# Performance work log

Measured on AMD Instinct MI355X. Metric: run time of the kernel, lower is better.

## Reference

```python
import jax, jax.numpy as jnp
import numpy as np
from jax import lax

RES = 14
DIM = 384
KEY_DIM = 32
NUM_HEADS = 12
ATTN_RATIO = 4
NH_KD = KEY_DIM * NUM_HEADS            # 384
DH = ATTN_RATIO * KEY_DIM * NUM_HEADS  # 1536
HQKV = DH + 2 * NH_KD                  # 2304
BN_EPS = 1e-5


def _bias_idxs():
    ys, xs = np.meshgrid(np.arange(RES), np.arange(RES), indexing='ij')
    ys = ys.reshape(-1); xs = xs.reshape(-1)
    dy = np.abs(ys[:, None] - ys[None, :])
    dx = np.abs(xs[:, None] - xs[None, :])
    return jnp.asarray(dy * RES + dx, dtype=jnp.int32)  # [196,196], 196 unique offsets


def setup_inputs() -> dict:
    key = jax.random.key(0)
    ks = jax.random.split(key, 16)
    B = 128
    x = jax.random.normal(ks[0], (B, DIM, RES, RES), dtype=jnp.float32)
    # qkv: 1x1 conv DIM->HQKV + BN
    qkv_w = jax.random.normal(ks[1], (HQKV, DIM, 1, 1), dtype=jnp.float32) * 0.05
    qkv_g = jax.random.normal(ks[2], (HQKV,), dtype=jnp.float32) * 0.1 + 1.0
    qkv_b = jax.random.normal(ks[3], (HQKV,), dtype=jnp.float32) * 0.1
    qkv_m = jax.random.normal(ks[4], (HQKV,), dtype=jnp.float32) * 0.1
    qkv_v = jax.random.uniform(ks[5], (HQKV,), dtype=jnp.float32) + 0.5
    # dw: depthwise 3x3 conv on q channels + BN
    dw_w = jax.random.normal(ks[6], (NH_KD, 1, 3, 3), dtype=jnp.float32) * 0.2
    dw_g = jax.random.normal(ks[7], (NH_KD,), dtype=jnp.float32) * 0.1 + 1.0
    dw_b = jax.random.normal(ks[8], (NH_KD,), dtype=jnp.float32) * 0.1
    dw_m = jax.random.normal(ks[9], (NH_KD,), dtype=jnp.float32) * 0.1
    dw_v = jax.random.uniform(ks[10], (NH_KD,), dtype=jnp.float32) + 0.5
    # proj: ReLU -> 1x1 conv DH->DIM + BN
    proj_w = jax.random.normal(ks[11], (DIM, DH, 1, 1), dtype=jnp.float32) * 0.05
    proj_g = jax.random.normal(ks[12], (DIM,), dtype=jnp.float32) * 0.1 + 1.0
    proj_b = jax.random.normal(ks[13], (DIM,), dtype=jnp.float32) * 0.1
    proj_m = jax.random.normal(ks[14], (DIM,), dtype=jnp.float32) * 0.1
    proj_v = jax.random.uniform(ks[15], (DIM,), dtype=jnp.float32) + 0.5
    ab = jax.random.normal(jax.random.fold_in(key, 99), (NUM_HEADS, RES * RES), dtype=jnp.float32) * 0.1
    return {
        'x': x,
        'qkv_w': qkv_w, 'qkv_g': qkv_g, 'qkv_b': qkv_b, 'qkv_m': qkv_m, 'qkv_v': qkv_v,
        'dw_w': dw_w, 'dw_g': dw_g, 'dw_b': dw_b, 'dw_m': dw_m, 'dw_v': dw_v,
        'proj_w': proj_w, 'proj_g': proj_g, 'proj_b': proj_b, 'proj_m': proj_m, 'proj_v': proj_v,
        'attn_biases': ab,
        'bias_idxs': _bias_idxs(),
    }


def _bn(x, g, b, m, v):
    scale = g / jnp.sqrt(v + BN_EPS)
    return x * scale[None, :, None, None] + (b - m * scale)[None, :, None, None]


def reference(x, qkv_w, qkv_g, qkv_b, qkv_m, qkv_v,
              dw_w, dw_g, dw_b, dw_m, dw_v,
              proj_w, proj_g, proj_b, proj_m, proj_v,
              attn_biases, bias_idxs):
    B, _, H, W = x.shape
    n = H * W
    scale = KEY_DIM ** -0.5
    # 1x1 conv + BN
    qkv = jnp.einsum('bchw,oc->bohw', x, qkv_w[:, :, 0, 0])
    qkv = _bn(qkv, qkv_g, qkv_b, qkv_m, qkv_v)
    q = qkv[:, :NH_KD]
    k = qkv[:, NH_KD:2 * NH_KD]
    v = qkv[:, 2 * NH_KD:]
    # depthwise 3x3 conv + BN on q
    q = lax.conv_general_dilated(q, dw_w, (1, 1), ((1, 1), (1, 1)),
                                 dimension_numbers=('NCHW', 'OIHW', 'NCHW'),
                                 feature_group_count=NH_KD)
    q = _bn(q, dw_g, dw_b, dw_m, dw_v)
    # heads: [b, h, d, n]
    q = q.reshape(B, NUM_HEADS, KEY_DIM, n)
    k = k.reshape(B, NUM_HEADS, KEY_DIM, n)
    v = v.reshape(B, NUM_HEADS, ATTN_RATIO * KEY_DIM, n)
    bias = attn_biases[:, bias_idxs]  # [h, n, n]
    attn = jnp.einsum('bhdn,bhdm->bhnm', q, k) * scale + bias[None]
    attn = jax.nn.softmax(attn, axis=-1)
    out = jnp.einsum('bhdm,bhnm->bhdn', v, attn).reshape(B, DH, H, W)
    out = jax.nn.relu(out)
    out = jnp.einsum('bchw,oc->bohw', out, proj_w[:, :, 0, 0])
    return _bn(out, proj_g, proj_b, proj_m, proj_v)
```

## Files before the change

kernel.cpp:

```cpp
#include <hip/hip_runtime.h>

typedef __bf16 bf16;
typedef bf16 bf16x8 __attribute__((ext_vector_type(8)));
typedef bf16 bf16x4 __attribute__((ext_vector_type(4)));
typedef short short4v __attribute__((ext_vector_type(4)));
typedef float f32x4 __attribute__((ext_vector_type(4)));

#define NPIX 196
#define CIN 384
#define NHEADS 12
#define MPAD 224
#define VSTRIDE 232
#define OSTRIDE 40
#define TSTRIDE 136

__device__ __forceinline__ float ldf(const void* p, size_t i, int f) {
    return f ? ((const float*)p)[i] : (float)((const bf16*)p)[i];
}

__device__ __forceinline__ void gld16(const void* g, void* lds_wave_base) {
    __builtin_amdgcn_global_load_lds(
        (const __attribute__((address_space(1))) void*)(unsigned long long)g,
        (__attribute__((address_space(3))) void*)(unsigned long long)lds_wave_base,
        16, 0, 0);
}

__device__ __forceinline__ int xcd_swizzle(int orig, int nwg) {
    int q = nwg >> 3, r = nwg & 7;
    int xcd = orig & 7, idx = orig >> 3;
    return (xcd < r ? xcd * (q + 1) : r * (q + 1) + (xcd - r) * q) + idx;
}

__device__ __forceinline__ f32x4 mfma16(bf16x4 a, bf16x4 b, f32x4 c) {
#if __has_builtin(__builtin_amdgcn_mfma_f32_16x16x16bf16_1k)
    return __builtin_amdgcn_mfma_f32_16x16x16bf16_1k(
        __builtin_bit_cast(short4v, a), __builtin_bit_cast(short4v, b), c, 0, 0, 0);
#else
    asm volatile("v_mfma_f32_16x16x16_bf16 %0, %1, %2, %0" : "+v"(c) : "v"(a), "v"(b));
    return c;
#endif
}

__device__ __forceinline__ f32x4 vmax4(f32x4 a, f32x4 b) {
    f32x4 r;
    r[0] = fmaxf(a[0], b[0]);
    r[1] = fmaxf(a[1], b[1]);
    r[2] = fmaxf(a[2], b[2]);
    r[3] = fmaxf(a[3], b[3]);
    return r;
}

__global__ void detect_kernel(const unsigned int* __restrict__ x, int* __restrict__ flag) {
    __shared__ int cnt;
    if (threadIdx.x == 0) cnt = 0;
    __syncthreads();
    int c = 0;
#pragma unroll
    for (int k = 0; k < 8; k++) {
        unsigned int w = x[threadIdx.x * 8 + k];
        unsigned int e = (w >> 7) & 0xFFu;
        if (e > 200u) c++;
    }
    atomicAdd(&cnt, c);
    __syncthreads();
    if (threadIdx.x == 0) *flag = (cnt >= 16) ? 1 : 0;
}

__global__ void convert_kernel(const void* __restrict__ src, bf16* __restrict__ dst, int n,
                               const int* __restrict__ flag) {
    int f = *flag;
    for (int i = blockIdx.x * 256 + threadIdx.x; i < n; i += gridDim.x * 256)
        dst[i] = (bf16)ldf(src, i, f);
}

__global__ void transpose_x_kernel(const void* __restrict__ x, const int* __restrict__ flag,
                                   bf16* __restrict__ xt, int b0) {
    __shared__ bf16 tile[32][33];
    int f = *flag;
    int b = blockIdx.z, gb = b0 + b;
    int c0 = blockIdx.y * 32;
    int hw0 = blockIdx.x * 32;
    int tx = threadIdx.x, ty = threadIdx.y;
    int hw = hw0 + tx, c = c0 + ty;
    if (hw < NPIX) tile[ty][tx] = (bf16)ldf(x, ((size_t)gb * CIN + c) * NPIX + hw, f);
    __syncthreads();
    int hw2 = hw0 + ty, c2 = c0 + tx;
    if (hw2 < NPIX) xt[((size_t)b * NPIX + hw2) * CIN + c2] = tile[tx][ty];
}

__device__ __forceinline__ void gemm_tile(const bf16* __restrict__ A, const bf16* __restrict__ B,
                                          int K, bf16* smem, f32x4 acc[4][4]) {
    int tid = threadIdx.x;
    int wave = tid >> 6, lane = tid & 63;
    int wm = wave >> 1, wn = wave & 1;
    int row = lane & 15, grp = lane >> 4;
    int sr = lane >> 3;
    int scg = (lane & 7) ^ sr;
    const int BUF = 128 * 64;
    bf16* As = smem;
    bf16* Bs = smem + 2 * BUF;
    const bf16* Ag = A + (size_t)(wave * 8 + sr) * K + scg * 8;
    const bf16* Bg = B + (size_t)(wave * 8 + sr) * K + scg * 8;
#pragma unroll
    for (int p = 0; p < 4; p++) {
        gld16(Ag + (size_t)(p * 32) * K, As + (p * 256 + wave * 64) * 8);
        gld16(Bg + (size_t)(p * 32) * K, Bs + (p * 256 + wave * 64) * 8);
    }
    int cur = 0;
#pragma unroll 1
    for (int kb = 0; kb < K; kb += 64) {
        if (kb + 64 < K) {
            bf16* Asn = As + (cur ^ 1) * BUF;
            bf16* Bsn = Bs + (cur ^ 1) * BUF;
#pragma unroll
            for (int p = 0; p < 4; p++) {
                gld16(Ag + (size_t)(p * 32) * K + kb + 64, Asn + (p * 256 + wave * 64) * 8);
                gld16(Bg + (size_t)(p * 32) * K + kb + 64, Bsn + (p * 256 + wave * 64) * 8);
            }
            __builtin_amdgcn_sched_barrier(0);
            asm volatile("s_waitcnt vmcnt(8)" ::: "memory");
        } else {
            __builtin_amdgcn_sched_barrier(0);
            asm volatile("s_waitcnt vmcnt(0)" ::: "memory");
        }
        __builtin_amdgcn_s_barrier();
        __builtin_amdgcn_sched_barrier(0);
        const bf16* Asc = As + cur * BUF;
        const bf16* Bsc = Bs + cur * BUF;
#pragma unroll
        for (int ki = 0; ki < 2; ki++) {
            bf16x8 af[4], bfr[4];
#pragma unroll
            for (int t = 0; t < 4; t++) {
                int ra = wm * 64 + t * 16 + row;
                af[t] = *(const bf16x8*)(Asc + ra * 64 + (((ki * 4 + grp) ^ (ra & 7)) * 8));
                int rb = wn * 64 + t * 16 + row;
                bfr[t] = *(const bf16x8*)(Bsc + rb * 64 + (((ki * 4 + grp) ^ (rb & 7)) * 8));
            }
#pragma unroll
            for (int mt = 0; mt < 4; mt++)
#pragma unroll
                for (int nt = 0; nt < 4; nt++)
                    acc[mt][nt] =
                        __builtin_amdgcn_mfma_f32_16x16x32_bf16(af[mt], bfr[nt], acc[mt][nt], 0, 0, 0);
        }
        __builtin_amdgcn_sched_barrier(0);
        __builtin_amdgcn_s_barrier();
        cur ^= 1;
    }
    __builtin_amdgcn_sched_barrier(0);
}

__global__ __launch_bounds__(256) void gemm_qkv_kernel(
    const bf16* __restrict__ xt, const bf16* __restrict__ w,
    const void* __restrict__ g, const void* __restrict__ bb,
    const void* __restrict__ mm, const void* __restrict__ vv, const int* __restrict__ flag,
    bf16* __restrict__ qb, bf16* __restrict__ kt, bf16* __restrict__ vb) {
    __shared__ bf16 smem[4 * 128 * 64];
    f32x4 acc[4][4];
#pragma unroll
    for (int i = 0; i < 4; i++)
#pragma unroll
        for (int j = 0; j < 4; j++) acc[i][j] = (f32x4){0.f, 0.f, 0.f, 0.f};
    int nwg = gridDim.x * gridDim.y;
    int l = xcd_swizzle(blockIdx.y * gridDim.x + blockIdx.x, nwg);
    int m0 = (l % gridDim.x) * 128, n0 = (l / gridDim.x) * 128;
    gemm_tile(w + (size_t)m0 * CIN, xt + (size_t)n0 * CIN, CIN, smem, acc);
    int f = *flag;
    int tid = threadIdx.x;
    int wave = tid >> 6, lane = tid & 63;
    int wm = wave >> 1, wn = wave & 1, row = lane & 15, grp = lane >> 4;
    if (m0 >= 384 && m0 < 768) {
        bf16* tbuf = smem;
#pragma unroll
        for (int mt = 0; mt < 4; mt++) {
#pragma unroll
            for (int r = 0; r < 4; r++) {
                int ol = wm * 64 + mt * 16 + grp * 4 + r;
                int o = m0 + ol;
                float scv = ldf(g, o, f) * rsqrtf(ldf(vv, o, f) + 1e-5f);
                float sh = ldf(bb, o, f) - ldf(mm, o, f) * scv;
#pragma unroll
                for (int nt = 0; nt < 4; nt++) {
                    int nl = wn * 64 + nt * 16 + row;
                    tbuf[nl * TSTRIDE + ol] = (bf16)(acc[mt][nt][r] * scv + sh);
                }
            }
        }
        __syncthreads();
#pragma unroll
        for (int it = 0; it < 8; it++) {
            int g2 = it * 256 + tid;
            int nl = g2 >> 4, ch = g2 & 15;
            *(bf16x8*)(kt + (size_t)(n0 + nl) * CIN + (m0 - 384) + ch * 8) =
                *(const bf16x8*)(tbuf + nl * TSTRIDE + ch * 8);
        }
    } else {
#pragma unroll
        for (int mt = 0; mt < 4; mt++) {
#pragma unroll
            for (int r = 0; r < 4; r++) {
                int o = m0 + wm * 64 + mt * 16 + grp * 4 + r;
                float scv = ldf(g, o, f) * rsqrtf(ldf(vv, o, f) + 1e-5f);
                float sh = ldf(bb, o, f) - ldf(mm, o, f) * scv;
#pragma unroll
                for (int nt = 0; nt < 4; nt++) {
                    int n = n0 + wn * 64 + nt * 16 + row;
                    int b = n / NPIX, hw = n - b * NPIX;
                    float val = acc[mt][nt][r] * scv + sh;
                    bf16 bv = (bf16)val;
                    if (o < 384) {
                        qb[((size_t)b * 384 + o) * NPIX + hw] = bv;
                    } else {
                        vb[((size_t)b * 1536 + (o - 768)) * MPAD + hw] = bv;
                    }
                }
            }
        }
    }
}

__global__ __launch_bounds__(256) void gemm_proj_kernel(
    const bf16* __restrict__ ot, const bf16* __restrict__ w,
    const void* __restrict__ g, const void* __restrict__ bb,
    const void* __restrict__ mm, const void* __restrict__ vv, const int* __restrict__ flag,
    void* __restrict__ out, int b0) {
    __shared__ bf16 smem[4 * 128 * 64];
    f32x4 acc[4][4];
#pragma unroll
    for (int i = 0; i < 4; i++)
#pragma unroll
        for (int j = 0; j < 4; j++) acc[i][j] = (f32x4){0.f, 0.f, 0.f, 0.f};
    int nwg = gridDim.x * gridDim.y;
    int l = xcd_swizzle(blockIdx.y * gridDim.x + blockIdx.x, nwg);
    int m0 = (l % gridDim.x) * 128, n0 = (l / gridDim.x) * 128;
    gemm_tile(w + (size_t)m0 * 1536, ot + (size_t)n0 * 1536, 1536, smem, acc);
    int f = *flag;
    int wave = threadIdx.x >> 6, lane = threadIdx.x & 63;
    int wm = wave >> 1, wn = wave & 1, row = lane & 15, grp = lane >> 4;
#pragma unroll
    for (int mt = 0; mt < 4; mt++) {
#pragma unroll
        for (int r = 0; r < 4; r++) {
            int o = m0 + wm * 64 + mt * 16 + grp * 4 + r;
            float scv = ldf(g, o, f) * rsqrtf(ldf(vv, o, f) + 1e-5f);
            float sh = ldf(bb, o, f) - ldf(mm, o, f) * scv;
#pragma unroll
            for (int nt = 0; nt < 4; nt++) {
                int n = n0 + wn * 64 + nt * 16 + row;
                int b = n / NPIX, hw = n - b * NPIX;
                float val = acc[mt][nt][r] * scv + sh;
                size_t oidx = ((size_t)(b0 + b) * 384 + o) * NPIX + hw;
                if (f) ((float*)out)[oidx] = val;
                else ((bf16*)out)[oidx] = (bf16)val;
            }
        }
    }
}

__global__ void dwconv_kernel(const bf16* __restrict__ qb, const bf16* __restrict__ w,
                              const void* __restrict__ g, const void* __restrict__ bb,
                              const void* __restrict__ mm, const void* __restrict__ vv,
                              const int* __restrict__ flag, bf16* __restrict__ qt) {
    __shared__ bf16 tile[32][33];
    int f = *flag;
    int b = blockIdx.z;
    int c0 = blockIdx.y * 32, hw0 = blockIdx.x * 32;
    int tx = threadIdx.x, ty = threadIdx.y;
    int c = c0 + ty, hw = hw0 + tx;
    if (hw < NPIX) {
        int y = hw / 14, x = hw % 14;
        float acc = 0.f;
        const bf16* wp = w + c * 9;
        const bf16* qp = qb + ((size_t)b * 384 + c) * NPIX;
#pragma unroll
        for (int ky = 0; ky < 3; ky++) {
            int yy = y + ky - 1;
            if (yy < 0 || yy >= 14) continue;
#pragma unroll
            for (int kx = 0; kx < 3; kx++) {
                int xx = x + kx - 1;
                if (xx < 0 || xx >= 14) continue;
                acc += (float)qp[yy * 14 + xx] * (float)wp[ky * 3 + kx];
            }
        }
        float sc = ldf(g, c, f) * rsqrtf(ldf(vv, c, f) + 1e-5f);
        float sh = ldf(bb, c, f) - ldf(mm, c, f) * sc;
        tile[ty][tx] = (bf16)(acc * sc + sh);
    }
    __syncthreads();
    int hw2 = hw0 + ty, c2 = c0 + tx;
    if (hw2 < NPIX) qt[((size_t)b * NPIX + hw2) * CIN + c2] = tile[tx][ty];
}

__global__ void bias_gather_kernel(const void* __restrict__ ab, const int* __restrict__ idx,
                                   const int* __restrict__ flag, float* __restrict__ biasf) {
    int f = *flag;
    int t = blockIdx.x * 256 + threadIdx.x;
    if (t >= NHEADS * NPIX * MPAD) return;
    int h = t / (NPIX * MPAD);
    int rem = t - h * (NPIX * MPAD);
    int n = rem / MPAD, m = rem - n * MPAD;
    biasf[t] = (m < NPIX) ? ldf(ab, h * NPIX + idx[n * NPIX + m], f) : -1e30f;
}

__global__ void zero_vpad_kernel(bf16* __restrict__ vb, int rows) {
    int t = blockIdx.x * 256 + threadIdx.x;
    if (t >= rows * 7) return;
    int r = t / 7, c = t - r * 7;
    *(unsigned long long*)(vb + (size_t)r * MPAD + NPIX + c * 4) = 0ull;
}

__global__ __launch_bounds__(256, 2) void attn_kernel(
    const bf16* __restrict__ qt, const bf16* __restrict__ ktp, const bf16* __restrict__ vb,
    const float* __restrict__ biasf, bf16* __restrict__ ot) {
    __shared__ bf16 Vs[128 * VSTRIDE];
    __shared__ bf16 Osh[4][16 * OSTRIDE];
    int nwg = gridDim.x * gridDim.y;
    int l = xcd_swizzle(blockIdx.y * gridDim.x + blockIdx.x, nwg);
    int h = l % NHEADS, b = l / NHEADS;
    int tid = threadIdx.x;
    int wave = tid >> 6, lane = tid & 63;
    int row = lane & 15, grp = lane >> 4;
    const float scale = 0.17677669529663687f;
    const f32x4 zf = {0.f, 0.f, 0.f, 0.f};

    {
        const bf16* vsrc = vb + ((size_t)b * 1536 + h * 128) * MPAD;
#pragma unroll
        for (int it = 0; it < 14; it++) {
            int i = it * 256 + tid;
            int r = i / 28, gch = i - r * 28;
            *(bf16x8*)(Vs + r * VSTRIDE + gch * 8) = *(const bf16x8*)(vsrc + (size_t)i * 8);
        }
    }
    __syncthreads();

    const bf16* vls = Vs + row * VSTRIDE + grp * 4;

    for (int nb = wave; nb < 13; nb += 4) {
        int n0 = nb * 16;
        int n = n0 + row;
        int nc = n > 195 ? 195 : n;

        bf16x8 aq = *(const bf16x8*)(qt + ((size_t)b * NPIX + nc) * CIN + h * 32 + grp * 8);

        f32x4 sacc[14];
#pragma unroll
        for (int mt = 0; mt < 14; mt++) {
            int krow = mt * 16 + row;
            if (krow > 195) krow = 195;
            bf16x8 ak = *(const bf16x8*)(ktp + ((size_t)b * NPIX + krow) * CIN + h * 32 + grp * 8);
            sacc[mt] = __builtin_amdgcn_mfma_f32_16x16x32_bf16(ak, aq, zf, 0, 0, 0);
        }

        const float* bp = biasf + ((size_t)h * NPIX + nc) * MPAD + grp * 4;
        f32x4 mxv = {-3.4e38f, -3.4e38f, -3.4e38f, -3.4e38f};
#pragma unroll
        for (int mt = 0; mt < 14; mt++) {
            f32x4 bv = *(const f32x4*)(bp + mt * 16);
            f32x4 s = sacc[mt] * scale + bv;
            sacc[mt] = s;
            mxv = vmax4(mxv, s);
        }
        float mx = fmaxf(fmaxf(mxv[0], mxv[1]), fmaxf(mxv[2], mxv[3]));
        mx = fmaxf(mx, __shfl_xor(mx, 16));
        mx = fmaxf(mx, __shfl_xor(mx, 32));

        f32x4 sumv = zf;
        bf16x4 pf[14];
#pragma unroll
        for (int mt = 0; mt < 14; mt++) {
            f32x4 e;
#pragma unroll
            for (int r = 0; r < 4; r++) e[r] = __expf(sacc[mt][r] - mx);
            sumv += e;
            bf16x4 pb;
#pragma unroll
            for (int r = 0; r < 4; r++) pb[r] = (bf16)e[r];
            pf[mt] = pb;
        }
        float sum = (sumv[0] + sumv[1]) + (sumv[2] + sumv[3]);
        sum += __shfl_xor(sum, 16);
        sum += __shfl_xor(sum, 32);
        float inv = 1.f / sum;

        f32x4 oacc[8];
#pragma unroll
        for (int dt = 0; dt < 8; dt++) oacc[dt] = zf;
#pragma unroll
        for (int mt = 0; mt < 14; mt++) {
            bf16x4 p = pf[mt];
#pragma unroll
            for (int dt = 0; dt < 8; dt++) {
                bf16x4 v4 = *(const bf16x4*)(vls + dt * 16 * VSTRIDE + mt * 16);
                oacc[dt] = mfma16(v4, p, oacc[dt]);
            }
        }

        bf16* osw = Osh[wave];
        int r2 = lane >> 2, c2 = lane & 3;
        int n2 = n0 + r2;
        bf16* op = ot + ((size_t)b * NPIX + n2) * 1536 + h * 128;
#pragma unroll
        for (int dp = 0; dp < 4; dp++) {
#pragma unroll
            for (int u = 0; u < 2; u++) {
                int dt = dp * 2 + u;
                bf16x4 o4;
#pragma unroll
                for (int r = 0; r < 4; r++) {
                    float v = oacc[dt][r] * inv;
                    o4[r] = (bf16)(v > 0.f ? v : 0.f);
                }
                *(bf16x4*)(osw + row * OSTRIDE + u * 16 + grp * 4) = o4;
            }
            asm volatile("s_waitcnt lgkmcnt(0)" ::: "memory");
            if (n2 < NPIX) {
                bf16x8 ov = *(const bf16x8*)(osw + r2 * OSTRIDE + c2 * 8);
                *(bf16x8*)(op + dp * 32 + c2 * 8) = ov;
            }
            asm volatile("s_waitcnt lgkmcnt(0)" ::: "memory");
        }
    }
}

extern "C" void kernel_launch(void* const* d_in, const int* in_sizes, int n_in,
                              void* d_out, int out_size, void* d_ws, size_t ws_size,
                              hipStream_t stream) {
    const void* x      = d_in[0];
    const void* qkv_w  = d_in[1];
    const void* qkv_g  = d_in[2];
    const void* qkv_b  = d_in[3];
    const void* qkv_m  = d_in[4];
    const void* qkv_v  = d_in[5];
    const void* dw_w   = d_in[6];
    const void* dw_g   = d_in[7];
    const void* dw_b   = d_in[8];
    const void* dw_m   = d_in[9];
    const void* dw_v   = d_in[10];
    const void* proj_w = d_in[11];
    const void* proj_g = d_in[12];
    const void* proj_b = d_in[13];
    const void* proj_m = d_in[14];
    const void* proj_v = d_in[15];
    const void* ab     = d_in[16];
    const int*  idx    = (const int*)d_in[17];

    char* ws = (char*)d_ws;
    size_t off = 0;
    auto alloc = [&](size_t bytes) { void* p = ws + off; off += (bytes + 255) & ~(size_t)255; return p; };

    int*   flag = (int*)alloc(4);
    bf16*  wq   = (bf16*)alloc((size_t)2304 * 384 * 2);
    bf16*  wp   = (bf16*)alloc((size_t)384 * 1536 * 2);
    bf16*  wd   = (bf16*)alloc((size_t)384 * 9 * 2);
    float* biasf= (float*)alloc((size_t)NHEADS * NPIX * MPAD * 4);
    size_t fixed = off;

    const size_t s_xt = (size_t)NPIX * CIN;
    const size_t s_qb = (size_t)384 * NPIX;
    const size_t s_kt = (size_t)NPIX * 384;
    const size_t s_vb = (size_t)1536 * MPAD;
    const size_t s_ot = (size_t)NPIX * 1536;
    const size_t per_image = (s_xt + s_qb + s_kt + s_vb + s_ot) * 2;

    int CB = 128;
    while (CB > 32 && fixed + (size_t)CB * per_image > ws_size) CB >>= 1;

    bf16* xt  = (bf16*)alloc((size_t)CB * s_xt * 2);
    bf16* qb  = (bf16*)alloc((size_t)CB * s_qb * 2);
    bf16* ktp = (bf16*)alloc((size_t)CB * s_kt * 2);
    bf16* vb  = (bf16*)alloc((size_t)CB * s_vb * 2);
    bf16* ot  = (bf16*)alloc((size_t)CB * s_ot * 2);
    bf16* qt  = xt;

    detect_kernel<<<dim3(1), dim3(256), 0, stream>>>((const unsigned int*)x, flag);
    convert_kernel<<<dim3(256), dim3(256), 0, stream>>>(qkv_w, wq, 2304 * 384, flag);
    convert_kernel<<<dim3(256), dim3(256), 0, stream>>>(proj_w, wp, 384 * 1536, flag);
    convert_kernel<<<dim3(4), dim3(256), 0, stream>>>(dw_w, wd, 384 * 9, flag);
    int bg = (NHEADS * NPIX * MPAD + 255) / 256;
    bias_gather_kernel<<<dim3(bg), dim3(256), 0, stream>>>(ab, idx, flag, biasf);
    int vrows = CB * 1536;
    zero_vpad_kernel<<<dim3((vrows * 7 + 255) / 256), dim3(256), 0, stream>>>(vb, vrows);

    dim3 tb(32, 32);
    for (int b0 = 0; b0 < 128; b0 += CB) {
        int cb = (128 - b0 < CB) ? (128 - b0) : CB;
        int ntiles = (cb * NPIX) / 128;
        transpose_x_kernel<<<dim3(7, 12, cb), tb, 0, stream>>>(x, flag, xt, b0);
        gemm_qkv_kernel<<<dim3(18, ntiles), dim3(256), 0, stream>>>(xt, wq, qkv_g, qkv_b, qkv_m,
                                                                    qkv_v, flag, qb, ktp, vb);
        dwconv_kernel<<<dim3(7, 12, cb), tb, 0, stream>>>(qb, wd, dw_g, dw_b, dw_m, dw_v, flag, qt);
        attn_kernel<<<dim3(NHEADS, cb), dim3(256), 0, stream>>>(qt, ktp, vb, biasf, ot);
        gemm_proj_kernel<<<dim3(3, ntiles), dim3(256), 0, stream>>>(ot, wp, proj_g, proj_b, proj_m,
                                                                    proj_v, flag, d_out, b0);
    }
}
```

Baseline: 446.9 us.

## Merge prep kernels, stage GEMM epilogues through LDS, add MFMA priority hints

```diff
diff --git a/kernel.cpp b/kernel.cpp
--- a/kernel.cpp
+++ b/kernel.cpp
@@ -13,6 +13,12 @@
 #define VSTRIDE 232
 #define OSTRIDE 40
 #define TSTRIDE 136
+#define TSF 136
+
+#define N_WQ (2304 * 384)
+#define N_WP (384 * 1536)
+#define N_WD (384 * 9)
+#define N_BI (NHEADS * NPIX * MPAD)
 
 __device__ __forceinline__ float ldf(const void* p, size_t i, int f) {
     return f ? ((const float*)p)[i] : (float)((const bf16*)p)[i];
@@ -66,11 +72,31 @@
     if (threadIdx.x == 0) *flag = (cnt >= 16) ? 1 : 0;
 }
 
-__global__ void convert_kernel(const void* __restrict__ src, bf16* __restrict__ dst, int n,
-                               const int* __restrict__ flag) {
+__global__ void prep_kernel(const void* __restrict__ qkv_w, const void* __restrict__ proj_w,
+                            const void* __restrict__ dw_w, const void* __restrict__ ab,
+                            const int* __restrict__ idx, const int* __restrict__ flag,
+                            bf16* __restrict__ wq, bf16* __restrict__ wp, bf16* __restrict__ wd,
+                            float* __restrict__ biasf, bf16* __restrict__ vb, int nvpad) {
     int f = *flag;
-    for (int i = blockIdx.x * 256 + threadIdx.x; i < n; i += gridDim.x * 256)
-        dst[i] = (bf16)ldf(src, i, f);
+    long t = (long)blockIdx.x * 256 + threadIdx.x;
+    if (t < N_WQ) { wq[t] = (bf16)ldf(qkv_w, t, f); return; }
+    t -= N_WQ;
+    if (t < N_WP) { wp[t] = (bf16)ldf(proj_w, t, f); return; }
+    t -= N_WP;
+    if (t < N_WD) { wd[t] = (bf16)ldf(dw_w, t, f); return; }
+    t -= N_WD;
+    if (t < N_BI) {
+        int h = (int)(t / (NPIX * MPAD));
+        int rem = (int)(t - (long)h * (NPIX * MPAD));
+        int n = rem / MPAD, m = rem - n * MPAD;
+        biasf[t] = (m < NPIX) ? ldf(ab, h * NPIX + idx[n * NPIX + m], f) : -1e30f;
+        return;
+    }
+    t -= N_BI;
+    if (t < nvpad) {
+        long r = t / 7, c = t - r * 7;
+        *(unsigned long long*)(vb + r * MPAD + NPIX + c * 4) = 0ull;
+    }
 }
 
 __global__ void transpose_x_kernel(const void* __restrict__ x, const int* __restrict__ flag,
@@ -170,8 +196,8 @@
     int tid = threadIdx.x;
     int wave = tid >> 6, lane = tid & 63;
     int wm = wave >> 1, wn = wave & 1, row = lane & 15, grp = lane >> 4;
+    bf16* tbuf = smem;
     if (m0 >= 384 && m0 < 768) {
-        bf16* tbuf = smem;
 #pragma unroll
         for (int mt = 0; mt < 4; mt++) {
 #pragma unroll
@@ -200,20 +226,41 @@
         for (int mt = 0; mt < 4; mt++) {
 #pragma unroll
             for (int r = 0; r < 4; r++) {
-                int o = m0 + wm * 64 + mt * 16 + grp * 4 + r;
+                int ol = wm * 64 + mt * 16 + grp * 4 + r;
+                int o = m0 + ol;
                 float scv = ldf(g, o, f) * rsqrtf(ldf(vv, o, f) + 1e-5f);
                 float sh = ldf(bb, o, f) - ldf(mm, o, f) * scv;
 #pragma unroll
                 for (int nt = 0; nt < 4; nt++) {
-                    int n = n0 + wn * 64 + nt * 16 + row;
-                    int b = n / NPIX, hw = n - b * NPIX;
-                    float val = acc[mt][nt][r] * scv + sh;
-                    bf16 bv = (bf16)val;
-                    if (o < 384) {
-                        qb[((size_t)b * 384 + o) * NPIX + hw] = bv;
-                    } else {
-                        vb[((size_t)b * 1536 + (o - 768)) * MPAD + hw] = bv;
-                    }
+                    int nl = wn * 64 + nt * 16 + row;
+                    tbuf[ol * TSTRIDE + nl] = (bf16)(acc[mt][nt][r] * scv + sh);
+                }
+            }
+        }
+        __syncthreads();
+        bool isq = (m0 < 384);
+        bf16* dst = isq ? qb : vb;
+        int ostride = isq ? NPIX : MPAD;
+        int obase = isq ? m0 : (m0 - 768);
+        int orow_mul = isq ? 384 : 1536;
+#pragma unroll
+        for (int it = 0; it < 8; it++) {
+            int g2 = it * 256 + tid;
+            int ol = g2 >> 4, ch = g2 & 15;
+            int o = obase + ol;
+            int ng = n0 + ch * 8;
+            int b0i = ng / NPIX, hw0 = ng - b0i * NPIX;
+            const bf16* src = tbuf + ol * TSTRIDE + ch * 8;
+            if (hw0 <= NPIX - 8) {
+                bf16* d = dst + ((size_t)b0i * orow_mul + o) * ostride + hw0;
+                *(bf16x4*)d = *(const bf16x4*)src;
+                *(bf16x4*)(d + 4) = *(const bf16x4*)(src + 4);
+            } else {
+#pragma unroll
+                for (int j = 0; j < 8; j++) {
+                    int n2 = ng + j;
+                    int bj = n2 / NPIX, hwj = n2 - bj * NPIX;
+                    dst[((size_t)bj * orow_mul + o) * ostride + hwj] = src[j];
                 }
             }
         }
@@ -236,23 +283,69 @@
     int m0 = (l % gridDim.x) * 128, n0 = (l / gridDim.x) * 128;
     gemm_tile(w + (size_t)m0 * 1536, ot + (size_t)n0 * 1536, 1536, smem, acc);
     int f = *flag;
-    int wave = threadIdx.x >> 6, lane = threadIdx.x & 63;
+    int tid = threadIdx.x;
+    int wave = tid >> 6, lane = tid & 63;
     int wm = wave >> 1, wn = wave & 1, row = lane & 15, grp = lane >> 4;
-#pragma unroll
-    for (int mt = 0; mt < 4; mt++) {
-#pragma unroll
-        for (int r = 0; r < 4; r++) {
-            int o = m0 + wm * 64 + mt * 16 + grp * 4 + r;
-            float scv = ldf(g, o, f) * rsqrtf(ldf(vv, o, f) + 1e-5f);
-            float sh = ldf(bb, o, f) - ldf(mm, o, f) * scv;
-#pragma unroll
-            for (int nt = 0; nt < 4; nt++) {
-                int n = n0 + wn * 64 + nt * 16 + row;
-                int b = n / NPIX, hw = n - b * NPIX;
-                float val = acc[mt][nt][r] * scv + sh;
-                size_t oidx = ((size_t)(b0 + b) * 384 + o) * NPIX + hw;
-                if (f) ((float*)out)[oidx] = val;
-                else ((bf16*)out)[oidx] = (bf16)val;
+    if (f) {
+        float* tb = (float*)smem;
+#pragma unroll
+        for (int half = 0; half < 2; half++) {
+            if (wm == half) {
+#pragma unroll
+                for (int mt = 0; mt < 4; mt++) {
+#pragma unroll
+                    for (int r = 0; r < 4; r++) {
+                        int ol = mt * 16 + grp * 4 + r;
+                        int o = m0 + half * 64 + ol;
+                        float scv = ldf(g, o, f) * rsqrtf(ldf(vv, o, f) + 1e-5f);
+                        float sh = ldf(bb, o, f) - ldf(mm, o, f) * scv;
+#pragma unroll
+                        for (int nt = 0; nt < 4; nt++) {
+                            int nl = wn * 64 + nt * 16 + row;
+                            tb[ol * TSF + nl] = acc[mt][nt][r] * scv + sh;
+                        }
+                    }
+                }
+            }
+            __syncthreads();
+            float* outf = (float*)out;
+#pragma unroll
+            for (int it = 0; it < 8; it++) {
+                int g2 = it * 256 + tid;
+                int ol = g2 >> 5, ch = g2 & 31;
+                int o = m0 + half * 64 + ol;
+                int ng = n0 + ch * 4;
+                int b0i = ng / NPIX, hw0 = ng - b0i * NPIX;
+                const float* src = tb + ol * TSF + ch * 4;
+                if (hw0 <= NPIX - 4) {
+                    *(f32x4*)(outf + ((size_t)(b0 + b0i) * 384 + o) * NPIX + hw0) =
+                        *(const f32x4*)src;
+                } else {
+#pragma unroll
+                    for (int j = 0; j < 4; j++) {
+                        int n2 = ng + j;
+                        int bj = n2 / NPIX, hwj = n2 - bj * NPIX;
+                        outf[((size_t)(b0 + bj) * 384 + o) * NPIX + hwj] = src[j];
+                    }
+                }
+            }
+            __syncthreads();
+        }
+    } else {
+#pragma unroll
+        for (int mt = 0; mt < 4; mt++) {
+#pragma unroll
+            for (int r = 0; r < 4; r++) {
+                int o = m0 + wm * 64 + mt * 16 + grp * 4 + r;
+                float scv = ldf(g, o, f) * rsqrtf(ldf(vv, o, f) + 1e-5f);
+                float sh = ldf(bb, o, f) - ldf(mm, o, f) * scv;
+#pragma unroll
+                for (int nt = 0; nt < 4; nt++) {
+                    int n = n0 + wn * 64 + nt * 16 + row;
+                    int b = n / NPIX, hw = n - b * NPIX;
+                    ((bf16*)out)[((size_t)(b0 + b) * 384 + o) * NPIX + hw] =
+                        (bf16)(acc[mt][nt][r] * scv + sh);
+                }
             }
         }
     }
@@ -293,24 +386,6 @@
     if (hw2 < NPIX) qt[((size_t)b * NPIX + hw2) * CIN + c2] = tile[tx][ty];
 }
 
-__global__ void bias_gather_kernel(const void* __restrict__ ab, const int* __restrict__ idx,
-                                   const int* __restrict__ flag, float* __restrict__ biasf) {
-    int f = *flag;
-    int t = blockIdx.x * 256 + threadIdx.x;
-    if (t >= NHEADS * NPIX * MPAD) return;
-    int h = t / (NPIX * MPAD);
-    int rem = t - h * (NPIX * MPAD);
-    int n = rem / MPAD, m = rem - n * MPAD;
-    biasf[t] = (m < NPIX) ? ldf(ab, h * NPIX + idx[n * NPIX + m], f) : -1e30f;
-}
-
-__global__ void zero_vpad_kernel(bf16* __restrict__ vb, int rows) {
-    int t = blockIdx.x * 256 + threadIdx.x;
-    if (t >= rows * 7) return;
-    int r = t / 7, c = t - r * 7;
-    *(unsigned long long*)(vb + (size_t)r * MPAD + NPIX + c * 4) = 0ull;
-}
-
 __global__ __launch_bounds__(256, 2) void attn_kernel(
     const bf16* __restrict__ qt, const bf16* __restrict__ ktp, const bf16* __restrict__ vb,
     const float* __restrict__ biasf, bf16* __restrict__ ot) {
@@ -346,6 +421,7 @@
         bf16x8 aq = *(const bf16x8*)(qt + ((size_t)b * NPIX + nc) * CIN + h * 32 + grp * 8);
 
         f32x4 sacc[14];
+        __builtin_amdgcn_s_setprio(1);
 #pragma unroll
         for (int mt = 0; mt < 14; mt++) {
             int krow = mt * 16 + row;
@@ -353,6 +429,7 @@
             bf16x8 ak = *(const bf16x8*)(ktp + ((size_t)b * NPIX + krow) * CIN + h * 32 + grp * 8);
             sacc[mt] = __builtin_amdgcn_mfma_f32_16x16x32_bf16(ak, aq, zf, 0, 0, 0);
         }
+        __builtin_amdgcn_s_setprio(0);
 
         const float* bp = biasf + ((size_t)h * NPIX + nc) * MPAD + grp * 4;
         f32x4 mxv = {-3.4e38f, -3.4e38f, -3.4e38f, -3.4e38f};
@@ -388,6 +465,7 @@
         f32x4 oacc[8];
 #pragma unroll
         for (int dt = 0; dt < 8; dt++) oacc[dt] = zf;
+        __builtin_amdgcn_s_setprio(1);
 #pragma unroll
         for (int mt = 0; mt < 14; mt++) {
             bf16x4 p = pf[mt];
@@ -397,6 +475,7 @@
                 oacc[dt] = mfma16(v4, p, oacc[dt]);
             }
         }
+        __builtin_amdgcn_s_setprio(0);
 
         bf16* osw = Osh[wave];
         int r2 = lane >> 2, c2 = lane & 3;
@@ -452,10 +531,10 @@
     auto alloc = [&](size_t bytes) { void* p = ws + off; off += (bytes + 255) & ~(size_t)255; return p; };
 
     int*   flag = (int*)alloc(4);
-    bf16*  wq   = (bf16*)alloc((size_t)2304 * 384 * 2);
-    bf16*  wp   = (bf16*)alloc((size_t)384 * 1536 * 2);
-    bf16*  wd   = (bf16*)alloc((size_t)384 * 9 * 2);
-    float* biasf= (float*)alloc((size_t)NHEADS * NPIX * MPAD * 4);
+    bf16*  wq   = (bf16*)alloc((size_t)N_WQ * 2);
+    bf16*  wp   = (bf16*)alloc((size_t)N_WP * 2);
+    bf16*  wd   = (bf16*)alloc((size_t)N_WD * 2);
+    float* biasf= (float*)alloc((size_t)N_BI * 4);
     size_t fixed = off;
 
     const size_t s_xt = (size_t)NPIX * CIN;
@@ -476,13 +555,11 @@
     bf16* qt  = xt;
 
     detect_kernel<<<dim3(1), dim3(256), 0, stream>>>((const unsigned int*)x, flag);
-    convert_kernel<<<dim3(256), dim3(256), 0, stream>>>(qkv_w, wq, 2304 * 384, flag);
-    convert_kernel<<<dim3(256), dim3(256), 0, stream>>>(proj_w, wp, 384 * 1536, flag);
-    convert_kernel<<<dim3(4), dim3(256), 0, stream>>>(dw_w, wd, 384 * 9, flag);
-    int bg = (NHEADS * NPIX * MPAD + 255) / 256;
-    bias_gather_kernel<<<dim3(bg), dim3(256), 0, stream>>>(ab, idx, flag, biasf);
-    int vrows = CB * 1536;
-    zero_vpad_kernel<<<dim3((vrows * 7 + 255) / 256), dim3(256), 0, stream>>>(vb, vrows);
+    int nvpad = CB * 1536 * 7;
+    long prep_total = (long)N_WQ + N_WP + N_WD + N_BI + nvpad;
+    int prep_blocks = (int)((prep_total + 255) / 256);
+    prep_kernel<<<dim3(prep_blocks), dim3(256), 0, stream>>>(qkv_w, proj_w, dw_w, ab, idx, flag,
+                                                             wq, wp, wd, biasf, vb, nvpad);
 
     dim3 tb(32, 32);
     for (int b0 = 0; b0 < 128; b0 += CB) {
```

New measurement: 428.5 us. -4.1%, faster.
